# Performance work log

Measured on AMD Instinct MI355X. Metric: run time of the kernel, lower is better.

The kernel has to match this reference:

```python
import jax, jax.numpy as jnp
import numpy as np

N = 100000   # nodes in batch
E = 1600000  # edges
H = 128      # hidden_channels
G = 500      # number of subgraphs (batch ids)
MAXZ = 1000  # max_z
L = 3        # num_layers


def setup_inputs() -> dict:
    key = jax.random.key(0)
    ks = jax.random.split(key, 12)
    s = 1.0 / np.sqrt(H)
    z = jax.random.randint(ks[0], (N,), 0, MAXZ)
    edge_index = jax.random.randint(ks[1], (2, E), 0, N)
    batch = jnp.repeat(jnp.arange(G), N // G)  # sorted graph ids, 200 nodes/graph
    edge_weight = jax.random.uniform(ks[2], (E,), jnp.float32)
    z_table = jax.random.normal(ks[3], (MAXZ, H), jnp.float32) * s
    conv_Ws = tuple(jax.random.normal(ks[4 + i], (H, H), jnp.float32) * s for i in range(L))
    conv_bs = tuple(jnp.zeros((H,), jnp.float32) for _ in range(L))
    lin1_W = jax.random.normal(ks[8], (H, H), jnp.float32) * s
    lin1_b = jnp.zeros((H,), jnp.float32)
    lin2_W = jax.random.normal(ks[9], (H, 1), jnp.float32) * s
    lin2_b = jnp.zeros((1,), jnp.float32)
    return dict(z=z, edge_index=edge_index, batch=batch, edge_weight=edge_weight,
                z_table=z_table, conv_Ws=conv_Ws, conv_bs=conv_bs,
                lin1_W=lin1_W, lin1_b=lin1_b, lin2_W=lin2_W, lin2_b=lin2_b)


def gcn_norm(edge_index, edge_weight, n):
    # add self loops (fill value 1) and symmetric normalization, as in PyG gcn_norm
    loop = jnp.arange(n)
    row = jnp.concatenate([edge_index[0], loop])
    col = jnp.concatenate([edge_index[1], loop])
    w = jnp.concatenate([edge_weight, jnp.ones((n,), edge_weight.dtype)])
    deg = jax.ops.segment_sum(w, col, num_segments=n)
    dinv = jnp.where(deg > 0, jax.lax.rsqrt(deg), 0.0)
    norm = dinv[row] * w * dinv[col]
    return row, col, norm


def gcn_conv(x, row, col, norm, W, b):
    xw = x @ W                                        # [N,H] GEMM first (PyG order)
    msg = norm[:, None] * xw[row]                     # gather + scale  [E+N, H]
    out = jax.ops.segment_sum(msg, col, num_segments=x.shape[0])  # scatter-add
    return out + b


def reference(z, edge_index, batch, edge_weight, z_table, conv_Ws, conv_bs,
              lin1_W, lin1_b, lin2_W, lin2_b):
    x = z_table[z]                                    # z embedding [N,H]
    row, col, norm = gcn_norm(edge_index, edge_weight, x.shape[0])
    for i in range(L - 1):
        x = jax.nn.relu(gcn_conv(x, row, col, norm, conv_Ws[i], conv_bs[i]))
        # dropout is identity in eval mode
    x = gcn_conv(x, row, col, norm, conv_Ws[-1], conv_bs[-1])
    # first occurrence of each graph id in sorted batch == center node indices
    center = jnp.searchsorted(batch, jnp.arange(G))
    h = x[center] * x[center + 1]                     # src * dst center pair
    h = jax.nn.relu(h @ lin1_W + lin1_b)
    return h @ lin2_W + lin2_b                        # [G,1]
```

## Files before the change

kernel.cpp:

```cpp
#include <hip/hip_runtime.h>
#include <hip/hip_bf16.h>

#define H 128
#define CAP 64
#define GBM 64
#define GBN 64
#define NSWEEP 8
#define CNT_SCALE 16777216.0
#define RSHIFT 17
#define RMASK  0x1FFFF

typedef __attribute__((ext_vector_type(8))) short bf16x8;
typedef __attribute__((ext_vector_type(4))) float f32x4;

__device__ __forceinline__ unsigned short f2b(float f) {
  __hip_bfloat16 h = __float2bfloat16(f);
  union { __hip_bfloat16 h; unsigned short u; } c; c.h = h; return c.u;
}
__device__ __forceinline__ float b2f(unsigned short u) {
  union { unsigned int i; float f; } c; c.i = (unsigned)u << 16; return c.f;
}


__global__ void k_fillb2(const int* __restrict__ row, const int* __restrict__ col,
                         const float* __restrict__ ew, double* __restrict__ dsum,
                         int2* __restrict__ elist, int E, int shift) {
  int e = blockIdx.x * 256 + threadIdx.x;
  if (e >= E) return;
  int c = col[e];
  if ((c >> shift) != (int)blockIdx.z) return;
  float w = ew[e];
  double old = atomicAdd(&dsum[c], (double)w + CNT_SCALE);
  int pos = (int)(old * (1.0 / CNT_SCALE));
  if (pos < CAP) elist[(size_t)c * CAP + pos] = make_int2(row[e], __float_as_int(w));
}

__global__ void k_dinv(const double* __restrict__ dsum, float* __restrict__ dinv,
                       int* __restrict__ cnt, int n) {
  int i = blockIdx.x * 256 + threadIdx.x;
  if (i >= n) return;
  double v = dsum[i];
  double c = floor(v * (1.0 / CNT_SCALE));
  double s = v - c * CNT_SCALE + 1.0;
  dinv[i] = (float)(1.0 / sqrt(s));
  cnt[i] = (int)c;
}

__global__ __launch_bounds__(256) void k_pack(const int* __restrict__ cnt,
    int* __restrict__ cntp, const float* __restrict__ dinv, const int* __restrict__ z,
    int2* __restrict__ elist, int n) {
  int wid = (blockIdx.x * 256 + threadIdx.x) >> 4;
  if (wid >= n) return;
  int lane = threadIdx.x & 15;
  int m = min(cnt[wid], CAP);
  int mp = (m + 7) & ~7;
  if (lane == 0) cntp[wid] = mp;
  float dc = dinv[wid];
  for (int j = lane; j < mp; j += 16) {
    size_t idx = (size_t)wid * CAP + j;
    if (j < m) {
      int2 e = elist[idx];
      int r = e.x;
      float nrm = dinv[r] * __int_as_float(e.y) * dc;
      elist[idx] = make_int2(r | (z[r] << RSHIFT), __float_as_int(nrm));
    } else {
      elist[idx] = make_int2(0, 0);
    }
  }
}

__global__ void k_wprep(const float* __restrict__ W, unsigned short* __restrict__ whl) {
  int i = blockIdx.x * 256 + threadIdx.x;
  if (i >= H * H) return;
  int k = i >> 7, n = i & 127;
  float w = W[i];
  unsigned short hi = f2b(w);
  whl[n * H + k] = hi;
  whl[H * H + n * H + k] = f2b(w - b2f(hi));
}


__global__ __launch_bounds__(256) void k_mark(const int* __restrict__ batch, int n,
    int* __restrict__ clist, const int2* __restrict__ elist, const int* __restrict__ cnt,
    unsigned int* __restrict__ bitmap, int nc) {
  int widx = (blockIdx.x * 256 + threadIdx.x) >> 6;
  if (widx >= nc) return;
  int lane = threadIdx.x & 63;
  int g = widx >> 1;
  int lo = 0, hi = n;
  while (lo < hi) { int mid = (lo + hi) >> 1; if (batch[mid] < g) lo = mid + 1; else hi = mid; }
  int v = lo + (widx & 1);
  if (lane == 0) {
    clist[widx] = v;
    atomicOr(&bitmap[v >> 5], 1u << (v & 31));
  }
  int m = min(cnt[v], CAP);
  if (lane < m) {
    int r = elist[(size_t)v * CAP + lane].x & RMASK;
    atomicOr(&bitmap[r >> 5], 1u << (r & 31));
  }
}

__global__ void k_compact(const unsigned int* __restrict__ bitmap,
                          int* __restrict__ slist, int* __restrict__ scount, int n) {
  int i = blockIdx.x * 256 + threadIdx.x;
  if (i >= n) return;
  if (bitmap[i >> 5] & (1u << (i & 31))) slist[atomicAdd(scount, 1)] = i;
}


#define FMA4(A, xs, wv) { A[0] = fmaf(xs, wv.x, A[0]); A[1] = fmaf(xs, wv.y, A[1]); \
                          A[2] = fmaf(xs, wv.z, A[2]); A[3] = fmaf(xs, wv.w, A[3]); }

__global__ __launch_bounds__(256, 2) void k_gemm(const float* __restrict__ X,
    const float* __restrict__ Wg, void* __restrict__ Yv, int Nrows,
    const float* __restrict__ bias, int relu, int outbf) {
  __shared__ float Ws[H][GBN + 4];
  int tid = threadIdx.x;
  int bm = blockIdx.x * GBM;
  int bn = blockIdx.y * GBN;
  for (int i = tid; i < H * (GBN / 4); i += 256) {
    int k = i >> 4, c4 = (i & 15) * 4;
    *(float4*)&Ws[k][c4] = *(const float4*)(Wg + k * H + bn + c4);
  }
  __syncthreads();
  int rg = tid >> 4, cg = tid & 15;
  int cg4 = cg * 4;
  int g0 = bm + rg * 4 + 0, g1 = g0 + 1, g2 = g0 + 2, g3 = g0 + 3;
  const float* xp0; const float* xp1; const float* xp2; const float* xp3;
  {
    int c0 = g0 < Nrows ? g0 : Nrows - 1;
    int c1 = g1 < Nrows ? g1 : Nrows - 1;
    int c2 = g2 < Nrows ? g2 : Nrows - 1;
    int c3 = g3 < Nrows ? g3 : Nrows - 1;
    xp0 = X + (size_t)c0 * H; xp1 = X + (size_t)c1 * H;
    xp2 = X + (size_t)c2 * H; xp3 = X + (size_t)c3 * H;
  }
  float a0[4] = {0,0,0,0}, a1[4] = {0,0,0,0}, a2[4] = {0,0,0,0}, a3[4] = {0,0,0,0};
  #pragma unroll 2
  for (int k = 0; k < H; k += 4) {
    float4 x0 = *(const float4*)(xp0 + k);
    float4 x1 = *(const float4*)(xp1 + k);
    float4 x2 = *(const float4*)(xp2 + k);
    float4 x3 = *(const float4*)(xp3 + k);
    float4 w0 = *(const float4*)&Ws[k + 0][cg4];
    float4 w1 = *(const float4*)&Ws[k + 1][cg4];
    float4 w2 = *(const float4*)&Ws[k + 2][cg4];
    float4 w3 = *(const float4*)&Ws[k + 3][cg4];
    FMA4(a0, x0.x, w0) FMA4(a0, x0.y, w1) FMA4(a0, x0.z, w2) FMA4(a0, x0.w, w3)
    FMA4(a1, x1.x, w0) FMA4(a1, x1.y, w1) FMA4(a1, x1.z, w2) FMA4(a1, x1.w, w3)
    FMA4(a2, x2.x, w0) FMA4(a2, x2.y, w1) FMA4(a2, x2.z, w2) FMA4(a2, x2.w, w3)
    FMA4(a3, x3.x, w0) FMA4(a3, x3.y, w1) FMA4(a3, x3.z, w2) FMA4(a3, x3.w, w3)
  }
  if (bias) {
    float4 bb = *(const float4*)(bias + bn + cg4);
    #pragma unroll
    for (int u = 0; u < 4; ++u) {
      a0[u] += ((const float*)&bb)[u]; a1[u] += ((const float*)&bb)[u];
      a2[u] += ((const float*)&bb)[u]; a3[u] += ((const float*)&bb)[u];
    }
  }
  if (relu) {
    #pragma unroll
    for (int u = 0; u < 4; ++u) {
      a0[u] = fmaxf(a0[u], 0.f); a1[u] = fmaxf(a1[u], 0.f);
      a2[u] = fmaxf(a2[u], 0.f); a3[u] = fmaxf(a3[u], 0.f);
    }
  }
  if (outbf) {
    unsigned short* Yb = (unsigned short*)Yv;
    ushort4 h0 = make_ushort4(f2b(a0[0]), f2b(a0[1]), f2b(a0[2]), f2b(a0[3]));
    ushort4 h1 = make_ushort4(f2b(a1[0]), f2b(a1[1]), f2b(a1[2]), f2b(a1[3]));
    ushort4 h2 = make_ushort4(f2b(a2[0]), f2b(a2[1]), f2b(a2[2]), f2b(a2[3]));
    ushort4 h3 = make_ushort4(f2b(a3[0]), f2b(a3[1]), f2b(a3[2]), f2b(a3[3]));
    if (g0 < Nrows) *(ushort4*)(Yb + (size_t)g0 * H + bn + cg4) = h0;
    if (g1 < Nrows) *(ushort4*)(Yb + (size_t)g1 * H + bn + cg4) = h1;
    if (g2 < Nrows) *(ushort4*)(Yb + (size_t)g2 * H + bn + cg4) = h2;
    if (g3 < Nrows) *(ushort4*)(Yb + (size_t)g3 * H + bn + cg4) = h3;
  } else {
    float* Y = (float*)Yv;
    if (g0 < Nrows) *(float4*)(Y + (size_t)g0 * H + bn + cg4) = make_float4(a0[0], a0[1], a0[2], a0[3]);
    if (g1 < Nrows) *(float4*)(Y + (size_t)g1 * H + bn + cg4) = make_float4(a1[0], a1[1], a1[2], a1[3]);
    if (g2 < Nrows) *(float4*)(Y + (size_t)g2 * H + bn + cg4) = make_float4(a2[0], a2[1], a2[2], a2[3]);
    if (g3 < Nrows) *(float4*)(Y + (size_t)g3 * H + bn + cg4) = make_float4(a3[0], a3[1], a3[2], a3[3]);
  }
}


#define MFMA_GRID 512

__global__ __launch_bounds__(256, 2) void k_gemm_mfma(const unsigned short* __restrict__ Xb,
    const unsigned short* __restrict__ WHL, unsigned short* __restrict__ Yb, int Nrows) {
  __shared__ unsigned short WsH[H * H];
  __shared__ unsigned short WsL[H * H];
  int tid = threadIdx.x;
  {
    const int4* src = (const int4*)WHL;
    int4* dH = (int4*)WsH;
    int4* dL = (int4*)WsL;
    for (int i = tid; i < 2048; i += 256) {
      dH[i] = src[i];
      dL[i] = src[2048 + i];
    }
  }
  __syncthreads();
  int lane = tid & 63, wave = tid >> 6;
  int mrow = lane & 15, h = lane >> 4;
  int ntile = (Nrows + 63) >> 6;
  for (int t = blockIdx.x; t < ntile; t += MFMA_GRID) {
    int Mbase = t * 64 + wave * 16;
    int arow = Mbase + mrow;
    if (arow >= Nrows) arow = Nrows - 1;
    const unsigned short* xr = Xb + (size_t)arow * H;
    bf16x8 a[4];
    #pragma unroll
    for (int kt = 0; kt < 4; ++kt)
      a[kt] = *(const bf16x8*)(xr + kt * 32 + h * 8);
    f32x4 acc[8];
    #pragma unroll
    for (int nt = 0; nt < 8; ++nt) acc[nt] = (f32x4){0.f, 0.f, 0.f, 0.f};
    #pragma unroll
    for (int nt = 0; nt < 8; ++nt) {
      #pragma unroll
      for (int kt = 0; kt < 4; ++kt) {
        int boff = (nt * 16 + mrow) * H + kt * 32 + h * 8;
        bf16x8 bh = *(const bf16x8*)(WsH + boff);
        bf16x8 bl = *(const bf16x8*)(WsL + boff);
        acc[nt] = __builtin_amdgcn_mfma_f32_16x16x32_bf16(a[kt], bh, acc[nt], 0, 0, 0);
        acc[nt] = __builtin_amdgcn_mfma_f32_16x16x32_bf16(a[kt], bl, acc[nt], 0, 0, 0);
      }
    }
    #pragma unroll
    for (int nt = 0; nt < 8; ++nt) {
      int ocol = nt * 16 + mrow;
      #pragma unroll
      for (int r = 0; r < 4; ++r) {
        int orow = Mbase + 4 * h + r;
        if (orow < Nrows) Yb[(size_t)orow * H + ocol] = f2b(acc[nt][r]);
      }
    }
  }
}


__global__ __launch_bounds__(256) void k_aggb_list(const unsigned short* __restrict__ XWB,
    const int2* __restrict__ elist, const int* __restrict__ cntp,
    const float* __restrict__ dinv, const float* __restrict__ bias,
    float* __restrict__ out, const int* __restrict__ slist,
    const int* __restrict__ scount, int relu) {
  int widx = (blockIdx.x * 256 + threadIdx.x) >> 5;
  if (widx >= *scount) return;
  int wid = slist[widx];
  int c4 = threadIdx.x & 31;
  const ushort4* xw4 = (const ushort4*)XWB;
  int m = cntp[wid];
  const int2* ep = elist + (size_t)wid * CAP;
  float dc = dinv[wid];
  float d2 = dc * dc;
  ushort4 s = xw4[(size_t)wid * 32 + c4];
  float4 acc = make_float4(d2 * b2f(s.x), d2 * b2f(s.y), d2 * b2f(s.z), d2 * b2f(s.w));
  for (int j0 = 0; j0 < m; j0 += 8) {
    int2 Ee[8];
    #pragma unroll
    for (int u = 0; u < 8; ++u) Ee[u] = ep[j0 + u];
    ushort4 V[8];
    #pragma unroll
    for (int u = 0; u < 8; ++u) V[u] = xw4[(size_t)(Ee[u].x & RMASK) * 32 + c4];
    #pragma unroll
    for (int u = 0; u < 8; ++u) {
      float nn = __int_as_float(Ee[u].y);
      acc.x = fmaf(nn, b2f(V[u].x), acc.x);
      acc.y = fmaf(nn, b2f(V[u].y), acc.y);
      acc.z = fmaf(nn, b2f(V[u].z), acc.z);
      acc.w = fmaf(nn, b2f(V[u].w), acc.w);
    }
  }
  float4 bb = ((const float4*)bias)[c4];
  acc.x += bb.x; acc.y += bb.y; acc.z += bb.z; acc.w += bb.w;
  if (relu) {
    acc.x = fmaxf(acc.x, 0.f); acc.y = fmaxf(acc.y, 0.f);
    acc.z = fmaxf(acc.z, 0.f); acc.w = fmaxf(acc.w, 0.f);
  }
  ((float4*)out)[(size_t)wid * 32 + c4] = acc;
}


#define EFMA(nn, vv) { acc.x = fmaf(nn, vv.x, acc.x); acc.y = fmaf(nn, vv.y, acc.y); \
                       acc.z = fmaf(nn, vv.z, acc.z); acc.w = fmaf(nn, vv.w, acc.w); }

__global__ __launch_bounds__(256) void k_agg_last(const float* __restrict__ X,
    const int2* __restrict__ elist, const int* __restrict__ cntp,
    const float* __restrict__ dinv, const int* __restrict__ clist,
    float* __restrict__ out, int nc) {
  int widx = (blockIdx.x * 256 + threadIdx.x) >> 5;
  if (widx >= nc) return;
  int v = clist[widx];
  int c4 = threadIdx.x & 31;
  const float4* x4 = (const float4*)X;
  int m = cntp[v];
  const int2* ep = elist + (size_t)v * CAP;
  float dc = dinv[v];
  float d2 = dc * dc;
  float4 s = x4[(size_t)v * 32 + c4];
  float4 acc = make_float4(d2 * s.x, d2 * s.y, d2 * s.z, d2 * s.w);
  for (int j0 = 0; j0 < m; j0 += 8) {
    int2 Ee[8];
    #pragma unroll
    for (int u = 0; u < 8; ++u) Ee[u] = ep[j0 + u];
    float4 V[8];
    #pragma unroll
    for (int u = 0; u < 8; ++u) V[u] = x4[(size_t)(Ee[u].x & RMASK) * 32 + c4];
    #pragma unroll
    for (int u = 0; u < 8; ++u) {
      float nn = __int_as_float(Ee[u].y);
      EFMA(nn, V[u])
    }
  }
  ((float4*)out)[(size_t)widx * 32 + c4] = acc;
}


__global__ __launch_bounds__(256) void k_agg_emb(const unsigned short* __restrict__ ZTW,
    const int* __restrict__ z, const int2* __restrict__ elist, const int* __restrict__ cntp,
    const float* __restrict__ dinv, const float* __restrict__ bias,
    unsigned short* __restrict__ out, int n) {
  int wid = (blockIdx.x * 256 + threadIdx.x) >> 5;
  if (wid >= n) return;
  int c4 = threadIdx.x & 31;
  const ushort4* zt4 = (const ushort4*)ZTW;
  int m = cntp[wid];
  const int2* ep = elist + (size_t)wid * CAP;
  float dc = dinv[wid];
  float d2 = dc * dc;
  ushort4 s = zt4[(size_t)z[wid] * 32 + c4];
  float4 acc = make_float4(d2 * b2f(s.x), d2 * b2f(s.y), d2 * b2f(s.z), d2 * b2f(s.w));
  for (int j0 = 0; j0 < m; j0 += 8) {
    int2 Ee[8];
    #pragma unroll
    for (int u = 0; u < 8; ++u) Ee[u] = ep[j0 + u];
    ushort4 V[8];
    #pragma unroll
    for (int u = 0; u < 8; ++u) V[u] = zt4[(size_t)((unsigned)Ee[u].x >> RSHIFT) * 32 + c4];
    #pragma unroll
    for (int u = 0; u < 8; ++u) {
      float nn = __int_as_float(Ee[u].y);
      acc.x = fmaf(nn, b2f(V[u].x), acc.x);
      acc.y = fmaf(nn, b2f(V[u].y), acc.y);
      acc.z = fmaf(nn, b2f(V[u].z), acc.z);
      acc.w = fmaf(nn, b2f(V[u].w), acc.w);
    }
  }
  float4 bb = ((const float4*)bias)[c4];
  ushort4 o = make_ushort4(f2b(fmaxf(acc.x + bb.x, 0.f)),
                           f2b(fmaxf(acc.y + bb.y, 0.f)),
                           f2b(fmaxf(acc.z + bb.z, 0.f)),
                           f2b(fmaxf(acc.w + bb.w, 0.f)));
  ((ushort4*)out)[(size_t)wid * 32 + c4] = o;
}


__global__ __launch_bounds__(128) void k_head_y(const float* __restrict__ Y,
    const float* __restrict__ W1, const float* __restrict__ b1,
    const float* __restrict__ W2, const float* __restrict__ b2,
    float* __restrict__ out, int G) {
  int g = blockIdx.x, t = threadIdx.x;
  __shared__ float hs[H];
  hs[t] = Y[(size_t)(2 * g) * H + t] * Y[(size_t)(2 * g + 1) * H + t];
  __syncthreads();
  float a = b1[t];
  #pragma unroll 8
  for (int k = 0; k < H; ++k) a = fmaf(hs[k], W1[k * H + t], a);
  a = fmaxf(a, 0.f);
  a *= W2[t];
  for (int off = 32; off > 0; off >>= 1) a += __shfl_down(a, off);
  __shared__ float wsum[2];
  if ((t & 63) == 0) wsum[t >> 6] = a;
  __syncthreads();
  if (t == 0) out[g] = wsum[0] + wsum[1] + b2[0];
}


extern "C" void kernel_launch(void* const* d_in, const int* in_sizes, int n_in,
                              void* d_out, int out_size, void* d_ws, size_t ws_size,
                              hipStream_t stream) {
  const int* z     = (const int*)d_in[0];
  const int* eidx  = (const int*)d_in[1];
  const int* batch = (const int*)d_in[2];
  const float* ew  = (const float*)d_in[3];
  const float* ztab= (const float*)d_in[4];
  const float *W0, *W1, *W2, *b0, *b1, *b2, *l1W, *l1b, *l2W, *l2b;
  if (n_in >= 15) {
    W0 = (const float*)d_in[5];  W1 = (const float*)d_in[6];  W2 = (const float*)d_in[7];
    b0 = (const float*)d_in[8];  b1 = (const float*)d_in[9];  b2 = (const float*)d_in[10];
    l1W = (const float*)d_in[11]; l1b = (const float*)d_in[12];
    l2W = (const float*)d_in[13]; l2b = (const float*)d_in[14];
  } else {
    const float* Wss = (const float*)d_in[5];
    W0 = Wss; W1 = Wss + H * H; W2 = Wss + 2 * H * H;
    const float* bs = (const float*)d_in[6];
    b0 = bs; b1 = bs + H; b2 = bs + 2 * H;
    l1W = (const float*)d_in[7]; l1b = (const float*)d_in[8];
    l2W = (const float*)d_in[9]; l2b = (const float*)d_in[10];
  }
  int N = in_sizes[0];
  int E = in_sizes[3];
  int ZTOT = in_sizes[4];
  int MAXZ = ZTOT / H;
  int G = out_size;
  float* fout = (float*)d_out;
  int NC = 2 * G;
  int MAXS = NC * (CAP + 1);

  size_t woff = 0;
  auto alloc = [&](size_t bytes) {
    void* p = (char*)d_ws + woff;
    woff += (bytes + 255) & ~(size_t)255;
    return p;
  };
  unsigned short* h1b   = (unsigned short*)alloc((size_t)N * H * 2);
  unsigned short* xwb   = (unsigned short*)alloc((size_t)N * H * 2);
  float*          bufB  = (float*)alloc((size_t)N * H * 4);
  double*         dsum  = (double*)alloc((size_t)N * 8);
  unsigned int*   bitmap= (unsigned int*)alloc(((size_t)N + 31) / 32 * 4);
  int*            scount= (int*)alloc(4);
  float*          dinv  = (float*)alloc((size_t)N * 4);
  int*            cnt   = (int*)alloc((size_t)N * 4);
  int*            cntp  = (int*)alloc((size_t)N * 4);
  unsigned short* ztw   = (unsigned short*)alloc((size_t)ZTOT * 2);
  unsigned short* whl   = (unsigned short*)alloc((size_t)2 * H * H * 2);
  int*            clist = (int*)alloc((size_t)NC * 4);
  int*            slist = (int*)alloc((size_t)MAXS * 4);
  float*          agg2  = (float*)alloc((size_t)NC * H * 4);
  float*          ybuf  = (float*)alloc((size_t)NC * H * 4);
  int2*           elist = (int2*)alloc((size_t)N * CAP * 8);

  const int* erow = eidx;
  const int* ecol = eidx + E;

  size_t zlen = ((size_t)N * 8 + 255 & ~(size_t)255) + ((((size_t)N + 31) / 32 * 4 + 255) & ~(size_t)255) + 256;
  hipMemsetAsync(dsum, 0, zlen, stream);

  int nb = (N + 255) / 256;
  int eb = ((E + 255) / 256 + NSWEEP - 1) / NSWEEP * NSWEEP;
  int qgrid = (N + 15) / 16;
  int hgrid = (N + 7) / 8;

  int shift = 0; while ((NSWEEP << shift) < N) ++shift;

  dim3 fgrid(eb, 1, NSWEEP);
  k_fillb2<<<fgrid, 256, 0, stream>>>(erow, ecol, ew, dsum, elist, E, shift);
  k_dinv<<<nb, 256, 0, stream>>>(dsum, dinv, cnt, N);
  k_pack<<<qgrid, 256, 0, stream>>>(cnt, cntp, dinv, z, elist, N);
  dim3 zgrid((MAXZ + GBM - 1) / GBM, H / GBN);
  k_gemm<<<zgrid, 256, 0, stream>>>(ztab, W0, ztw, MAXZ, nullptr, 0, 1);
  k_wprep<<<(H * H + 255) / 256, 256, 0, stream>>>(W1, whl);
  k_mark<<<(NC + 3) / 4, 256, 0, stream>>>(batch, N, clist, elist, cnt, bitmap, NC);
  k_compact<<<nb, 256, 0, stream>>>(bitmap, slist, scount, N);

  k_agg_emb<<<hgrid, 256, 0, stream>>>(ztw, z, elist, cntp, dinv, b0, h1b, N);
  k_gemm_mfma<<<MFMA_GRID, 256, 0, stream>>>(h1b, whl, xwb, N);
  k_aggb_list<<<(MAXS + 7) / 8, 256, 0, stream>>>(xwb, elist, cntp, dinv, b1, bufB, slist, scount, 1);
  k_agg_last<<<(NC + 7) / 8, 256, 0, stream>>>(bufB, elist, cntp, dinv, clist, agg2, NC);
  dim3 ygrid((NC + GBM - 1) / GBM, H / GBN);
  k_gemm<<<ygrid, 256, 0, stream>>>(agg2, W2, ybuf, NC, b2, 0, 0);

  k_head_y<<<G, 128, 0, stream>>>(ybuf, l1W, l1b, l2W, l2b, fout, G);
}
```

Before: 268.7 us.

## Replace global double-atomic edge fill with two-pass shared-memory binning by column

Edge-list construction moves from one global double atomicAdd per edge (packed count and weight sum, run as 8 sweeps) to a two-pass bucket sort. The first pass builds a per-block histogram in shared memory and reserves bin space with one global atomic per bin. The second pass computes degree, dinv and the per-node CSR lists with shared-memory atomics inside each 128-node bin. This removes contended global fp64 atomics and the extra sweeps, at the cost of an intermediate binned buffer and a fixed per-bin cap of 4096 that silently clamps overflowing bins. Degree is now summed in fp32 and edge order within each node list becomes nondeterministic.

```diff
diff --git a/kernel.cpp b/kernel.cpp
--- a/kernel.cpp
+++ b/kernel.cpp
@@ -5,13 +5,16 @@
 #define CAP 64
 #define GBM 64
 #define GBN 64
-#define NSWEEP 8
-#define CNT_SCALE 16777216.0
+#define BW 128
+#define BSH 7
+#define BCAP 4096
+#define EPB 2048
 #define RSHIFT 17
 #define RMASK  0x1FFFF
 
 typedef __attribute__((ext_vector_type(8))) short bf16x8;
 typedef __attribute__((ext_vector_type(4))) float f32x4;
+typedef unsigned long long u64;
 
 __device__ __forceinline__ unsigned short f2b(float f) {
   __hip_bfloat16 h = __float2bfloat16(f);
@@ -22,28 +25,77 @@
 }
 
 
-__global__ void k_fillb2(const int* __restrict__ row, const int* __restrict__ col,
-                         const float* __restrict__ ew, double* __restrict__ dsum,
-                         int2* __restrict__ elist, int E, int shift) {
-  int e = blockIdx.x * 256 + threadIdx.x;
-  if (e >= E) return;
-  int c = col[e];
-  if ((c >> shift) != (int)blockIdx.z) return;
-  float w = ew[e];
-  double old = atomicAdd(&dsum[c], (double)w + CNT_SCALE);
-  int pos = (int)(old * (1.0 / CNT_SCALE));
-  if (pos < CAP) elist[(size_t)c * CAP + pos] = make_int2(row[e], __float_as_int(w));
-}
-
-__global__ void k_dinv(const double* __restrict__ dsum, float* __restrict__ dinv,
-                       int* __restrict__ cnt, int n) {
-  int i = blockIdx.x * 256 + threadIdx.x;
-  if (i >= n) return;
-  double v = dsum[i];
-  double c = floor(v * (1.0 / CNT_SCALE));
-  double s = v - c * CNT_SCALE + 1.0;
-  dinv[i] = (float)(1.0 / sqrt(s));
-  cnt[i] = (int)c;
+__global__ __launch_bounds__(256) void k_binA(const int* __restrict__ row,
+    const int* __restrict__ col, const float* __restrict__ ew,
+    int* __restrict__ gcur, u64* __restrict__ binned, int E, int NB) {
+  __shared__ int hist[1024];
+  __shared__ int gbase[1024];
+  int tid = threadIdx.x;
+  for (int i = tid; i < NB; i += 256) hist[i] = 0;
+  __syncthreads();
+  int base = blockIdx.x * EPB;
+  for (int j = tid; j < EPB; j += 256) {
+    int e = base + j;
+    if (e < E) atomicAdd(&hist[col[e] >> BSH], 1);
+  }
+  __syncthreads();
+  for (int i = tid; i < NB; i += 256) {
+    gbase[i] = atomicAdd(&gcur[i], hist[i]);
+    hist[i] = 0;
+  }
+  __syncthreads();
+  for (int j = tid; j < EPB; j += 256) {
+    int e = base + j;
+    if (e < E) {
+      int c = col[e];
+      int b = c >> BSH;
+      int r = atomicAdd(&hist[b], 1);
+      int pos = gbase[b] + r;
+      if (pos >= BCAP) pos = BCAP - 1;
+      unsigned pk = (unsigned)(c & (BW - 1)) | ((unsigned)row[e] << BSH);
+      binned[(size_t)b * BCAP + pos] = (u64)pk | ((u64)(unsigned)__float_as_int(ew[e]) << 32);
+    }
+  }
+}
+
+
+__global__ __launch_bounds__(256) void k_binB(const int* __restrict__ gcur,
+    const u64* __restrict__ binned, int* __restrict__ cnt, float* __restrict__ dinv,
+    int2* __restrict__ elist, int n) {
+  __shared__ int lcnt[BW];
+  __shared__ float lws[BW];
+  __shared__ int lcur[BW];
+  int b = blockIdx.x, tid = threadIdx.x;
+  if (tid < BW) { lcnt[tid] = 0; lws[tid] = 0.f; lcur[tid] = 0; }
+  __syncthreads();
+  int m = gcur[b];
+  if (m > BCAP) m = BCAP;
+  const u64* src = binned + (size_t)b * BCAP;
+  for (int j = tid; j < m; j += 256) {
+    u64 v = src[j];
+    int cl = (int)(v & (BW - 1));
+    atomicAdd(&lcnt[cl], 1);
+    atomicAdd(&lws[cl], __int_as_float((int)(v >> 32)));
+  }
+  __syncthreads();
+  if (tid < BW) {
+    int c = b * BW + tid;
+    if (c < n) {
+      cnt[c] = min(lcnt[tid], CAP);
+      dinv[c] = 1.f / sqrtf(1.f + lws[tid]);
+    }
+  }
+  __syncthreads();
+  for (int j = tid; j < m; j += 256) {
+    u64 v = src[j];
+    int cl = (int)(v & (BW - 1));
+    int r = atomicAdd(&lcur[cl], 1);
+    if (r < CAP) {
+      int c = b * BW + cl;
+      int rw = (int)((v >> BSH) & RMASK);
+      elist[(size_t)c * CAP + r] = make_int2(rw, (int)(v >> 32));
+    }
+  }
 }
 
 __global__ __launch_bounds__(256) void k_pack(const int* __restrict__ cnt,
@@ -410,6 +462,7 @@
   float* fout = (float*)d_out;
   int NC = 2 * G;
   int MAXS = NC * (CAP + 1);
+  int NB = (N + BW - 1) >> BSH;
 
   size_t woff = 0;
   auto alloc = [&](size_t bytes) {
@@ -420,9 +473,9 @@
   unsigned short* h1b   = (unsigned short*)alloc((size_t)N * H * 2);
   unsigned short* xwb   = (unsigned short*)alloc((size_t)N * H * 2);
   float*          bufB  = (float*)alloc((size_t)N * H * 4);
-  double*         dsum  = (double*)alloc((size_t)N * 8);
   unsigned int*   bitmap= (unsigned int*)alloc(((size_t)N + 31) / 32 * 4);
   int*            scount= (int*)alloc(4);
+  int*            gcur  = (int*)alloc((size_t)NB * 4);
   float*          dinv  = (float*)alloc((size_t)N * 4);
   int*            cnt   = (int*)alloc((size_t)N * 4);
   int*            cntp  = (int*)alloc((size_t)N * 4);
@@ -432,24 +485,22 @@
   int*            slist = (int*)alloc((size_t)MAXS * 4);
   float*          agg2  = (float*)alloc((size_t)NC * H * 4);
   float*          ybuf  = (float*)alloc((size_t)NC * H * 4);
+  u64*            binned= (u64*)alloc((size_t)NB * BCAP * 8);
   int2*           elist = (int2*)alloc((size_t)N * CAP * 8);
 
   const int* erow = eidx;
   const int* ecol = eidx + E;
 
-  size_t zlen = ((size_t)N * 8 + 255 & ~(size_t)255) + ((((size_t)N + 31) / 32 * 4 + 255) & ~(size_t)255) + 256;
-  hipMemsetAsync(dsum, 0, zlen, stream);
+  size_t zlen = ((((size_t)N + 31) / 32 * 4 + 255) & ~(size_t)255) + 256
+              + (((size_t)NB * 4 + 255) & ~(size_t)255);
+  hipMemsetAsync(bitmap, 0, zlen, stream);
 
   int nb = (N + 255) / 256;
-  int eb = ((E + 255) / 256 + NSWEEP - 1) / NSWEEP * NSWEEP;
   int qgrid = (N + 15) / 16;
   int hgrid = (N + 7) / 8;
 
-  int shift = 0; while ((NSWEEP << shift) < N) ++shift;
-
-  dim3 fgrid(eb, 1, NSWEEP);
-  k_fillb2<<<fgrid, 256, 0, stream>>>(erow, ecol, ew, dsum, elist, E, shift);
-  k_dinv<<<nb, 256, 0, stream>>>(dsum, dinv, cnt, N);
+  k_binA<<<(E + EPB - 1) / EPB, 256, 0, stream>>>(erow, ecol, ew, gcur, binned, E, NB);
+  k_binB<<<NB, 256, 0, stream>>>(gcur, binned, cnt, dinv, elist, N);
   k_pack<<<qgrid, 256, 0, stream>>>(cnt, cntp, dinv, z, elist, N);
   dim3 zgrid((MAXZ + GBM - 1) / GBM, H / GBN);
   k_gemm<<<zgrid, 256, 0, stream>>>(ztab, W0, ztw, MAXZ, nullptr, 0, 1);
```

New measurement: 248.4 us. 1.08x faster.
